# Optimization experiments

Hardware: AMD Instinct MI355X
Metric: run time of the kernel (lower is better)

The kernel has to match this reference:

```python
import jax, jax.numpy as jnp
import numpy as np

EPSILON = 0.1   # attention threshold
LN_EPS = 1e-5   # torch LayerNorm default
NORM_EPS = 1e-12  # torch F.normalize default


def setup_inputs() -> dict:
    key = jax.random.key(0)
    k1, k2, k3 = jax.random.split(key, 3)
    B, N, D = 4, 4096, 512
    Dqk, Dv = 512, 512
    x = jax.random.normal(k1, (B, N, D), dtype=jnp.float32)
    # xavier_uniform for Linear(in_dim, out_dim): bound = sqrt(6/(in+out))
    bqk = float(np.sqrt(6.0 / (D + Dqk)))
    bv = float(np.sqrt(6.0 / (D + Dv)))
    W_qk = jax.random.uniform(k2, (Dqk, D), minval=-bqk, maxval=bqk, dtype=jnp.float32)
    W_v = jax.random.uniform(k3, (Dv, D), minval=-bv, maxval=bv, dtype=jnp.float32)
    gamma = jnp.ones((Dv,), dtype=jnp.float32)
    beta = jnp.zeros((Dv,), dtype=jnp.float32)
    return {"x": x, "W_qk": W_qk, "W_v": W_v, "gamma": gamma, "beta": beta}


def reference(x, W_qk, W_v, gamma, beta):
    # q and k share the same projection (proj_qk applied twice to x)
    q = jnp.einsum('bnd,ed->bne', x, W_qk)   # [B,N,Dqk]
    v = jnp.einsum('bnd,ed->bne', x, W_v)    # [B,N,Dv]
    # L2 normalize (torch F.normalize: x / max(||x||, eps))
    qn = q / jnp.maximum(jnp.linalg.norm(q, axis=-1, keepdims=True), NORM_EPS)
    # cosine-similarity attention [B,N,N]
    attn = jnp.einsum('bne,bme->bnm', qn, qn)
    # epsilon-thresholded mask (detached in torch; constant here too)
    mask = jax.lax.stop_gradient((attn > EPSILON).astype(attn.dtype))
    attn = attn * mask  # markoff value is 0
    out = jnp.einsum('bnm,bme->bne', attn, v)  # [B,N,Dv]
    # LayerNorm over last dim
    mean = jnp.mean(out, axis=-1, keepdims=True)
    var = jnp.var(out, axis=-1, keepdims=True)
    out = (out - mean) * jax.lax.rsqrt(var + LN_EPS) * gamma + beta
    return out
```

## Files before the change

kernel.cpp:

```cpp
#include <hip/hip_runtime.h>
#include <hip/hip_bf16.h>
#include <stdint.h>


typedef __bf16 bf16;
typedef __bf16 bf16x8 __attribute__((ext_vector_type(8)));
typedef _Float16 f16;
typedef _Float16 f16x8 __attribute__((ext_vector_type(8)));
typedef unsigned short u16x8 __attribute__((ext_vector_type(8)));
typedef float f4 __attribute__((ext_vector_type(4)));
typedef float f16v __attribute__((ext_vector_type(16)));

#define CAP2 512
#define QBAND 2e-4f
#define BCAPC 512

#define SPLIT_HL(v0, v1, h, l)                                              \
    do {                                                                    \
        h[0] = (f16)v0.x; l[0] = (f16)((v0.x - (float)h[0]) * 2048.0f);     \
        h[1] = (f16)v0.y; l[1] = (f16)((v0.y - (float)h[1]) * 2048.0f);     \
        h[2] = (f16)v0.z; l[2] = (f16)((v0.z - (float)h[2]) * 2048.0f);     \
        h[3] = (f16)v0.w; l[3] = (f16)((v0.w - (float)h[3]) * 2048.0f);     \
        h[4] = (f16)v1.x; l[4] = (f16)((v1.x - (float)h[4]) * 2048.0f);     \
        h[5] = (f16)v1.y; l[5] = (f16)((v1.y - (float)h[5]) * 2048.0f);     \
        h[6] = (f16)v1.z; l[6] = (f16)((v1.z - (float)h[6]) * 2048.0f);     \
        h[7] = (f16)v1.w; l[7] = (f16)((v1.w - (float)h[7]) * 2048.0f);     \
    } while (0)

__global__ __launch_bounds__(512) void proj_q16(const float* __restrict__ X,
                                                const float* __restrict__ W,
                                                float* __restrict__ Q) {
    __shared__ f16 Bh[2][128][128];
    __shared__ f16 Bl[2][128][128];
    const int t = threadIdx.x;
    const int wave = t >> 6, lane = t & 63;
    const int ln16 = lane & 15, hi4 = lane >> 4;
    const int rg = wave >> 1, mg = wave & 1;
    const int n0 = blockIdx.x * 64;

    f16x8 Ah[16], Al[16];
    {
        const size_t arow = (size_t)(n0 + rg * 16 + ln16) * 512;
#pragma unroll
        for (int s = 0; s < 16; ++s) {
            f4 x0 = *(const f4*)&X[arow + s * 32 + hi4 * 8];
            f4 x1 = *(const f4*)&X[arow + s * 32 + hi4 * 8 + 4];
            f16x8 h, l;
            SPLIT_HL(x0, x1, h, l);
            Ah[s] = h; Al[s] = l;
        }
    }

#pragma unroll
    for (int i = 0; i < 4; ++i) {
        int id = i * 512 + t, r = id >> 4, s = id & 15;
        f4 w0 = *(const f4*)&W[(size_t)r * 512 + s * 8];
        f4 w1 = *(const f4*)&W[(size_t)r * 512 + s * 8 + 4];
        f16x8 h, l;
        SPLIT_HL(w0, w1, h, l);
        *(f16x8*)&Bh[0][r][(s ^ (r & 15)) * 8] = h;
        *(f16x8*)&Bl[0][r][(s ^ (r & 15)) * 8] = l;
    }
    __syncthreads();

    for (int ch = 0; ch < 4; ++ch) {
        const int eb = ch * 128;
        f4 Shh[4] = {}, Smid[4] = {};
#pragma unroll
        for (int k0i = 0; k0i < 4; ++k0i) {
            const int buf = k0i & 1;
            const bool last = (ch == 3) && (k0i == 3);
            const int neb = (k0i < 3) ? eb : eb + 128;
            const int nkb = (k0i < 3) ? (k0i + 1) * 128 : 0;
            f4 Lw[8];
            if (!last) {
#pragma unroll
                for (int i = 0; i < 4; ++i) {
                    int id = i * 512 + t, r = id >> 4, s = id & 15;
                    Lw[i * 2]     = *(const f4*)&W[(size_t)(neb + r) * 512 + nkb + s * 8];
                    Lw[i * 2 + 1] = *(const f4*)&W[(size_t)(neb + r) * 512 + nkb + s * 8 + 4];
                }
            }
#pragma unroll
            for (int kk = 0; kk < 4; ++kk) {
                const int s = k0i * 4 + kk;
                const f16x8 ah = Ah[s], al = Al[s];
#pragma unroll
                for (int tt = 0; tt < 4; ++tt) {
                    const int br = mg * 64 + tt * 16 + ln16;
                    const int sl = ((kk * 4 + hi4) ^ ln16) * 8;
                    f16x8 bh = *(const f16x8*)&Bh[buf][br][sl];
                    f16x8 bl = *(const f16x8*)&Bl[buf][br][sl];
                    Shh[tt]  = __builtin_amdgcn_mfma_f32_16x16x32_f16(ah, bh, Shh[tt], 0, 0, 0);
                    Smid[tt] = __builtin_amdgcn_mfma_f32_16x16x32_f16(al, bh, Smid[tt], 0, 0, 0);
                    Smid[tt] = __builtin_amdgcn_mfma_f32_16x16x32_f16(ah, bl, Smid[tt], 0, 0, 0);
                }
            }
            __syncthreads();
            if (!last) {
#pragma unroll
                for (int i = 0; i < 4; ++i) {
                    int id = i * 512 + t, r = id >> 4, s = id & 15;
                    f4 w0 = Lw[i * 2], w1 = Lw[i * 2 + 1];
                    f16x8 h, l;
                    SPLIT_HL(w0, w1, h, l);
                    *(f16x8*)&Bh[buf ^ 1][r][(s ^ (r & 15)) * 8] = h;
                    *(f16x8*)&Bl[buf ^ 1][r][(s ^ (r & 15)) * 8] = l;
                }
            }
            __syncthreads();
        }
#pragma unroll
        for (int tt = 0; tt < 4; ++tt) {
            const int ecol = eb + mg * 64 + tt * 16 + ln16;
#pragma unroll
            for (int i = 0; i < 4; ++i)
                Q[(size_t)(n0 + rg * 16 + hi4 * 4 + i) * 512 + ecol] =
                    Shh[tt][i] + Smid[tt][i] * (1.0f / 2048.0f);
        }
    }
}

__global__ __launch_bounds__(256) void proj_v16(const float* __restrict__ X,
                                                const float* __restrict__ W,
                                                bf16* __restrict__ VT) {
    __shared__ f16 Xs[128][256];
    const int t = threadIdx.x;
    const int wave = t >> 6, lane = t & 63;
    const int lo = lane & 15, h = lane >> 4;
    const int m0g = blockIdx.x * 128;
    const int e0 = blockIdx.y * 64;
    const int b = m0g >> 12, ml = m0g & 4095;

    f16x8 A[16];
    {
        const size_t arow = (size_t)(e0 + wave * 16 + lo) * 512;
#pragma unroll
        for (int s = 0; s < 16; ++s) {
            f4 w0 = *(const f4*)&W[arow + s * 32 + h * 8];
            f4 w1 = *(const f4*)&W[arow + s * 32 + h * 8 + 4];
            f16x8 a;
            a[0] = (f16)w0.x; a[1] = (f16)w0.y; a[2] = (f16)w0.z; a[3] = (f16)w0.w;
            a[4] = (f16)w1.x; a[5] = (f16)w1.y; a[6] = (f16)w1.z; a[7] = (f16)w1.w;
            A[s] = a;
        }
    }

    f4 acc[8] = {};
    for (int ph = 0; ph < 2; ++ph) {
        __syncthreads();
#pragma unroll
        for (int i = 0; i < 16; ++i) {
            int id = i * 256 + t;
            int r = id >> 5, s8 = id & 31;
            f4 x0 = *(const f4*)&X[(size_t)(m0g + r) * 512 + ph * 256 + s8 * 8];
            f4 x1 = *(const f4*)&X[(size_t)(m0g + r) * 512 + ph * 256 + s8 * 8 + 4];
            f16x8 v;
            v[0] = (f16)x0.x; v[1] = (f16)x0.y; v[2] = (f16)x0.z; v[3] = (f16)x0.w;
            v[4] = (f16)x1.x; v[5] = (f16)x1.y; v[6] = (f16)x1.z; v[7] = (f16)x1.w;
            int sl = (s8 & 16) | ((s8 ^ r) & 15);
            *(f16x8*)&Xs[r][sl * 8] = v;
        }
        __syncthreads();
#pragma unroll
        for (int s = 0; s < 8; ++s) {
            const f16x8 a = A[ph * 8 + s];
#pragma unroll
            for (int jt = 0; jt < 8; ++jt) {
                int rr = jt * 16 + lo;
                int c8 = s * 4 + h;
                int sl = (c8 & 16) | ((c8 ^ rr) & 15);
                f16x8 bb = *(const f16x8*)&Xs[rr][sl * 8];
                acc[jt] = __builtin_amdgcn_mfma_f32_16x16x32_f16(a, bb, acc[jt], 0, 0, 0);
            }
        }
    }
#pragma unroll
    for (int jt = 0; jt < 8; ++jt)
#pragma unroll
        for (int r = 0; r < 4; ++r) {
            int e = e0 + wave * 16 + h * 4 + r;
            int m = ml + jt * 16 + lo;
            VT[((size_t)b * 512 + e) * 4096 + m] = (bf16)acc[jt][r];
        }
}

__global__ __launch_bounds__(256) void norm_q(float* __restrict__ Q,
                                              f16* __restrict__ QH) {
    const int wave = threadIdx.x >> 6, lane = threadIdx.x & 63;
    const int row = blockIdx.x * 4 + wave;
    float* q = Q + (size_t)row * 512;
    float x[8];
    double s = 0.0;
    for (int j = 0; j < 8; ++j) { x[j] = q[lane * 8 + j]; s += (double)x[j] * x[j]; }
    for (int off = 1; off < 64; off <<= 1) s += __shfl_xor(s, off);
    double nm = fmax(sqrt(s), 1e-12);
    for (int j = 0; j < 8; ++j) {
        float qf = (float)((double)x[j] / nm);
        q[lane * 8 + j] = qf;
        QH[(size_t)row * 512 + lane * 8 + j] = (f16)qf;
    }
}

__global__ __launch_bounds__(512) void qk_mfma(const float* __restrict__ QF,
                                               const f16* __restrict__ QHB,
                                               uint16_t* __restrict__ counts,
                                               uint16_t* __restrict__ idxs,
                                               bf16* __restrict__ vals) {
    __shared__ f16 Bs[2][128][128];
    __shared__ int cnt[128];
    __shared__ int bcnt;
    __shared__ uint32_t blist[BCAPC];

    const int t = threadIdx.x;
    const int wave = t >> 6, lane = t & 63;
    const int ln16 = lane & 15, hi4 = lane >> 4;
    const int rg = wave >> 1, mg = wave & 1;
    const int grp = blockIdx.x & 7;
    const int b = grp >> 1, half = grp & 1;
    const int n0 = (blockIdx.x >> 3) * 128;
    const size_t nb = (size_t)b * 4096;
    const float* qf = QF + nb * 512;
    const f16* qh = QHB + nb * 512;
    const int mbase = half * 2048;

    f16x8 A[2][16];
#pragma unroll
    for (int rt = 0; rt < 2; ++rt) {
        const size_t arow = (size_t)(n0 + rg * 32 + rt * 16 + ln16) * 512;
#pragma unroll
        for (int s = 0; s < 16; ++s)
            A[rt][s] = *(const f16x8*)&qh[arow + s * 32 + hi4 * 8];
    }

    if (t < 128) cnt[t] = 0;
    if (t == 0) bcnt = 0;

#pragma unroll
    for (int i = 0; i < 4; ++i) {
        int id = i * 512 + t, r = id >> 4, s = id & 15;
        *(f16x8*)&Bs[0][r][(s ^ (r & 15)) * 8] =
            *(const f16x8*)&qh[(size_t)(mbase + r) * 512 + s * 8];
    }
    __syncthreads();

    for (int ch = 0; ch < 16; ++ch) {
        const int mst = mbase + ch * 128;
        f4 S[2][4] = {};
#pragma unroll
        for (int k0i = 0; k0i < 4; ++k0i) {
            const int buf = k0i & 1;
            const bool last = (k0i == 3) && (ch == 15);
            const int nmst = (k0i < 3) ? mst : mst + 128;
            const int nk0 = (k0i < 3) ? (k0i + 1) * 128 : 0;
            f16x8 L[4];
            if (!last) {
#pragma unroll
                for (int i = 0; i < 4; ++i) {
                    int id = i * 512 + t, r = id >> 4, s = id & 15;
                    L[i] = *(const f16x8*)&qh[(size_t)(nmst + r) * 512 + nk0 + s * 8];
                }
            }
#pragma unroll
            for (int kk = 0; kk < 4; ++kk) {
                const int s = k0i * 4 + kk;
                const f16x8 a0 = A[0][s], a1 = A[1][s];
#pragma unroll
                for (int tt = 0; tt < 4; ++tt) {
                    const int br = mg * 64 + tt * 16 + ln16;
                    f16x8 bb = *(const f16x8*)&Bs[buf][br][((kk * 4 + hi4) ^ ln16) * 8];
                    S[0][tt] = __builtin_amdgcn_mfma_f32_16x16x32_f16(a0, bb, S[0][tt], 0, 0, 0);
                    S[1][tt] = __builtin_amdgcn_mfma_f32_16x16x32_f16(a1, bb, S[1][tt], 0, 0, 0);
                }
            }
            if (k0i == 3) {
#pragma unroll
                for (int rt = 0; rt < 2; ++rt)
#pragma unroll
                    for (int tt = 0; tt < 4; ++tt) {
                        const int m = mst + mg * 64 + tt * 16 + ln16;
#pragma unroll
                        for (int i = 0; i < 4; ++i) {
                            float cs = S[rt][tt][i];
                            int row = rg * 32 + rt * 16 + hi4 * 4 + i;
                            if (cs > 0.1f + QBAND) {
                                int pos = atomicAdd(&cnt[row], 1);
                                if (pos < CAP2) {
                                    size_t o = ((size_t)(nb + n0 + row) * 2 + half) * CAP2 + pos;
                                    idxs[o] = (uint16_t)m;
                                    vals[o] = (bf16)cs;
                                }
                            } else if (cs > 0.1f - QBAND) {
                                int bp = atomicAdd(&bcnt, 1);
                                if (bp < BCAPC)
                                    blist[bp] = ((uint32_t)row << 12) | (uint32_t)m;
                            }
                        }
                    }
            }
            __syncthreads();
            if (!last) {
#pragma unroll
                for (int i = 0; i < 4; ++i) {
                    int id = i * 512 + t, r = id >> 4, s = id & 15;
                    *(f16x8*)&Bs[buf ^ 1][r][(s ^ (r & 15)) * 8] = L[i];
                }
            }
            if (k0i == 3) {
                int nbd = bcnt; if (nbd > BCAPC) nbd = BCAPC;
                for (int p = wave; p < nbd; p += 8) {
                    uint32_t pk = blist[p];
                    int row = (int)(pk >> 12), m = (int)(pk & 4095);
                    const float* qa = qf + (size_t)(n0 + row) * 512;
                    const float* qc = qf + (size_t)m * 512;
                    f4 a0 = *(const f4*)&qa[lane * 8];
                    f4 a1 = *(const f4*)&qa[lane * 8 + 4];
                    f4 c0 = *(const f4*)&qc[lane * 8];
                    f4 c1 = *(const f4*)&qc[lane * 8 + 4];
                    double s = (double)a0.x * c0.x + (double)a0.y * c0.y +
                               (double)a0.z * c0.z + (double)a0.w * c0.w +
                               (double)a1.x * c1.x + (double)a1.y * c1.y +
                               (double)a1.z * c1.z + (double)a1.w * c1.w;
                    for (int off = 1; off < 64; off <<= 1) s += __shfl_xor(s, off);
                    if (lane == 0 && s > 0.1) {
                        int pos = atomicAdd(&cnt[row], 1);
                        if (pos < CAP2) {
                            size_t o = ((size_t)(nb + n0 + row) * 2 + half) * CAP2 + pos;
                            idxs[o] = (uint16_t)m;
                            vals[o] = (bf16)(float)s;
                        }
                    }
                }
            }
            __syncthreads();
            if (k0i == 3 && t == 0) bcnt = 0;
        }
    }
    __syncthreads();
    if (t < 128) {
        int c = cnt[t];
        counts[(size_t)(nb + n0 + t) * 2 + half] = (uint16_t)(c > CAP2 ? CAP2 : c);
    }
}

__global__ __launch_bounds__(512, 2) void pv_mfma(const bf16* __restrict__ VT,
                                                  const uint16_t* __restrict__ counts,
                                                  const uint16_t* __restrict__ idxs,
                                                  const bf16* __restrict__ vals,
                                                  const float* __restrict__ gamma,
                                                  const float* __restrict__ beta,
                                                  float* __restrict__ Out) {
    __shared__ __align__(16) char smemraw[147456];
    bf16 (*Vts)[128] = (bf16(*)[128])smemraw;
    bf16 (*Wsm)[128] = (bf16(*)[128])(smemraw + 131072);

    const int t = threadIdx.x;
    const int wave = t >> 6, lane = t & 63;
    const int l31 = lane & 31, l15 = lane & 15, g = lane >> 5;
    const int grp = blockIdx.x & 7;
    const int b = grp >> 1;
    const int n0 = ((blockIdx.x >> 3) + ((grp & 1) ? 32 : 0)) * 64;
    const size_t nb = (size_t)b * 4096;
    const bf16* vtb = VT + (size_t)b * 512 * 4096;

    int myc0 = 0, myc1 = 0, cu = 0, pb = 0;
    u16x8 pi0 = {}, pi1 = {};
    bf16x8 pv0 = {}, pv1 = {};
    size_t base0 = 0, base1 = 0;
    if (t < 64) {
        myc0 = (int)counts[(size_t)(nb + n0 + t) * 2 + 0];
        myc1 = (int)counts[(size_t)(nb + n0 + t) * 2 + 1];
        if (myc0 > CAP2) myc0 = CAP2;
        if (myc1 > CAP2) myc1 = CAP2;
        base0 = ((size_t)(nb + n0 + t) * 2 + 0) * CAP2;
        base1 = ((size_t)(nb + n0 + t) * 2 + 1) * CAP2;
        pi0 = *(const u16x8*)&idxs[base0];
        pi1 = *(const u16x8*)&idxs[base0 + 8];
        pv0 = *(const bf16x8*)&vals[base0];
        pv1 = *(const bf16x8*)&vals[base0 + 8];
    }

    bf16x8 L[16];
#pragma unroll
    for (int i = 0; i < 16; ++i) {
        int id = i * 512 + t, r = id >> 4, s = id & 15;
        L[i] = *(const bf16x8*)&vtb[(size_t)r * 4096 + s * 8];
    }

    f16v acc[2][2] = {};

    for (int ch = 0; ch < 32; ++ch) {
        __syncthreads();
#pragma unroll
        for (int i = 0; i < 16; ++i) {
            int id = i * 512 + t, r = id >> 4, s = id & 15;
            *(bf16x8*)&Vts[r][(s ^ (r & 15)) << 3] = L[i];
        }
        if (t < 64) {
            bf16 z0 = (bf16)0.0f;
            bf16x8 zv = {z0, z0, z0, z0, z0, z0, z0, z0};
#pragma unroll
            for (int sj = 0; sj < 16; ++sj) *(bf16x8*)&Wsm[t][sj * 8] = zv;
            if (ch == 16) cu = 0;
            const int m0l = ch * 128;
            const int myc = (ch >= 16) ? myc1 : myc0;
            const size_t base = (ch >= 16) ? base1 : base0;
            int end = cu;
#pragma unroll
            for (int j = 0; j < 16; ++j) {
                int pos = pb + j;
                int mi = (j < 8) ? (int)pi0[j] : (int)pi1[j - 8];
                bf16 vv = (j < 8) ? pv0[j] : pv1[j - 8];
                if (pos == end && pos < myc && mi < m0l + 128) {
                    int lo = mi - m0l;
                    Wsm[t][(((lo >> 3) ^ (t & 15)) << 3) | (lo & 7)] = vv;
                    end = pos + 1;
                }
            }
            if (end == pb + 16) {
                while (end < myc) {
                    int mi = (int)idxs[base + end];
                    if (mi >= m0l + 128) break;
                    int lo = mi - m0l;
                    Wsm[t][(((lo >> 3) ^ (t & 15)) << 3) | (lo & 7)] =
                        vals[base + end];
                    ++end;
                }
            }
            cu = end;
        }
        __syncthreads();
        if (ch < 31) {
            const int mo = (ch + 1) * 128;
#pragma unroll
            for (int i = 0; i < 16; ++i) {
                int id = i * 512 + t, r = id >> 4, s = id & 15;
                L[i] = *(const bf16x8*)&vtb[(size_t)r * 4096 + mo + s * 8];
            }
            if (t < 64) {
                int ncu = (ch + 1 == 16) ? 0 : cu;
                const size_t nbase = (ch + 1 >= 16) ? base1 : base0;
                pb = ncu & ~7;
                pi0 = *(const u16x8*)&idxs[nbase + pb];
                pi1 = *(const u16x8*)&idxs[nbase + pb + 8];
                pv0 = *(const bf16x8*)&vals[nbase + pb];
                pv1 = *(const bf16x8*)&vals[nbase + pb + 8];
            }
        }
#pragma unroll
        for (int ks = 0; ks < 8; ++ks) {
            const int sw = (((ks * 2 + g) ^ l15) << 3);
            bf16x8 A0 = *(const bf16x8*)&Wsm[l31][sw];
            bf16x8 A1 = *(const bf16x8*)&Wsm[32 + l31][sw];
            bf16x8 B0 = *(const bf16x8*)&Vts[wave * 64 + l31][sw];
            bf16x8 B1 = *(const bf16x8*)&Vts[wave * 64 + 32 + l31][sw];
            acc[0][0] = __builtin_amdgcn_mfma_f32_32x32x16_bf16(A0, B0, acc[0][0], 0, 0, 0);
            acc[0][1] = __builtin_amdgcn_mfma_f32_32x32x16_bf16(A0, B1, acc[0][1], 0, 0, 0);
            acc[1][0] = __builtin_amdgcn_mfma_f32_32x32x16_bf16(A1, B0, acc[1][0], 0, 0, 0);
            acc[1][1] = __builtin_amdgcn_mfma_f32_32x32x16_bf16(A1, B1, acc[1][1], 0, 0, 0);
        }
    }

    __syncthreads();
    float* red = (float*)smemraw;
    float* mrs = (float*)(smemraw + 4096);
#pragma unroll
    for (int nt = 0; nt < 2; ++nt)
#pragma unroll
        for (int r = 0; r < 16; ++r) {
            float v0 = acc[nt][0][r], v1 = acc[nt][1][r];
            float s = v0 + v1, q = v0 * v0 + v1 * v1;
            for (int off = 1; off < 32; off <<= 1) {
                s += __shfl_xor(s, off);
                q += __shfl_xor(q, off);
            }
            if (l31 == 0) {
                int nloc = nt * 32 + (r & 3) + 8 * (r >> 2) + 4 * g;
                red[(wave * 64 + nloc) * 2] = s;
                red[(wave * 64 + nloc) * 2 + 1] = q;
            }
        }
    __syncthreads();
    if (t < 64) {
        float s = 0.f, q = 0.f;
        for (int w2 = 0; w2 < 8; ++w2) {
            s += red[(w2 * 64 + t) * 2];
            q += red[(w2 * 64 + t) * 2 + 1];
        }
        float mu = s * (1.0f / 512.0f);
        float var = q * (1.0f / 512.0f) - mu * mu;
        mrs[t] = mu;
        mrs[64 + t] = rsqrtf(var + 1e-5f);
    }
    __syncthreads();
    const float g0 = gamma[wave * 64 + l31], g1 = gamma[wave * 64 + 32 + l31];
    const float b0 = beta[wave * 64 + l31], b1 = beta[wave * 64 + 32 + l31];
#pragma unroll
    for (int nt = 0; nt < 2; ++nt)
#pragma unroll
        for (int r = 0; r < 16; ++r) {
            int nloc = nt * 32 + (r & 3) + 8 * (r >> 2) + 4 * g;
            float mu = mrs[nloc], rs = mrs[64 + nloc];
            size_t ro = (nb + n0 + nloc) * 512;
            float y0 = (acc[nt][0][r] - mu) * rs * g0 + b0;
            float y1 = (acc[nt][1][r] - mu) * rs * g1 + b1;
            Out[ro + wave * 64 + l31] = y0;
            Out[ro + wave * 64 + 32 + l31] = y1;
        }
}

extern "C" void kernel_launch(void* const* d_in, const int* in_sizes, int n_in,
                              void* d_out, int out_size, void* d_ws, size_t ws_size,
                              hipStream_t stream) {
    const float* x     = (const float*)d_in[0];
    const float* wqk   = (const float*)d_in[1];
    const float* wv    = (const float*)d_in[2];
    const float* gamma = (const float*)d_in[3];
    const float* beta  = (const float*)d_in[4];
    float* out = (float*)d_out;

    char* ws = (char*)d_ws;
    uint16_t* idxs   = (uint16_t*)ws;
    bf16*     vals   = (bf16*)(ws + 33554432);
    float*    qn32   = (float*)(ws + 67108864);
    f16*      qh16   = (f16*)(ws + 100663296);
    bf16*     vt     = (bf16*)(ws + 134217728);
    uint16_t* counts = (uint16_t*)(ws + 150994944);
    const size_t need = 151060480;
    if (ws_size < need) return;

    proj_q16<<<256, 512, 0, stream>>>(x, wqk, qn32);
    proj_v16<<<dim3(128, 8), 256, 0, stream>>>(x, wv, vt);
    norm_q<<<4096, 256, 0, stream>>>(qn32, qh16);
    qk_mfma<<<256, 512, 0, stream>>>(qn32, qh16, counts, idxs, vals);
    pv_mfma<<<256, 512, 0, stream>>>(vt, counts, idxs, vals, gamma, beta, out);
}
```

Baseline: 490.0 us.

## Split PV kernel across output-column halves and finish LayerNorm in separate kernel

The PV kernel now launches twice as many blocks, each computing only half of the 512 output columns for a 64-row tile, which halves the shared-memory footprint and the V tile loads per block. Partial row sums and sums of squares go to a workspace buffer, and a new ln_fin kernel combines them and applies the LayerNorm. The aim is more parallelism and better occupancy on the many-CU GPU. In exchange, each block redoes the sparse weight tile construction, and the unnormalised output takes an extra round trip through global memory plus one more kernel launch.

```diff
diff --git a/kernel.cpp b/kernel.cpp
--- a/kernel.cpp
+++ b/kernel.cpp
@@ -343,25 +343,25 @@
     }
 }
 
-__global__ __launch_bounds__(512, 2) void pv_mfma(const bf16* __restrict__ VT,
-                                                  const uint16_t* __restrict__ counts,
-                                                  const uint16_t* __restrict__ idxs,
-                                                  const bf16* __restrict__ vals,
-                                                  const float* __restrict__ gamma,
-                                                  const float* __restrict__ beta,
-                                                  float* __restrict__ Out) {
-    __shared__ __align__(16) char smemraw[147456];
+__global__ __launch_bounds__(512) void pv_mfma(const bf16* __restrict__ VT,
+                                               const uint16_t* __restrict__ counts,
+                                               const uint16_t* __restrict__ idxs,
+                                               const bf16* __restrict__ vals,
+                                               float* __restrict__ O,
+                                               float* __restrict__ sums) {
+    __shared__ __align__(16) char smemraw[81920];
     bf16 (*Vts)[128] = (bf16(*)[128])smemraw;
-    bf16 (*Wsm)[128] = (bf16(*)[128])(smemraw + 131072);
+    bf16 (*Wsm)[128] = (bf16(*)[128])(smemraw + 65536);
 
     const int t = threadIdx.x;
     const int wave = t >> 6, lane = t & 63;
     const int l31 = lane & 31, l15 = lane & 15, g = lane >> 5;
     const int grp = blockIdx.x & 7;
-    const int b = grp >> 1;
-    const int n0 = ((blockIdx.x >> 3) + ((grp & 1) ? 32 : 0)) * 64;
+    const int b = grp >> 1, eh = grp & 1;
+    const int n0 = (blockIdx.x >> 3) * 64;
+    const int e0 = eh * 256;
     const size_t nb = (size_t)b * 4096;
-    const bf16* vtb = VT + (size_t)b * 512 * 4096;
+    const bf16* vtb = VT + ((size_t)b * 512 + e0) * 4096;
 
     int myc0 = 0, myc1 = 0, cu = 0, pb = 0;
     u16x8 pi0 = {}, pi1 = {};
@@ -380,19 +380,20 @@
         pv1 = *(const bf16x8*)&vals[base0 + 8];
     }
 
-    bf16x8 L[16];
-#pragma unroll
-    for (int i = 0; i < 16; ++i) {
+    bf16x8 L[8];
+#pragma unroll
+    for (int i = 0; i < 8; ++i) {
         int id = i * 512 + t, r = id >> 4, s = id & 15;
         L[i] = *(const bf16x8*)&vtb[(size_t)r * 4096 + s * 8];
     }
 
-    f16v acc[2][2] = {};
+    const int nt = wave & 1, q = wave >> 1;
+    f16v acc[2] = {};
 
     for (int ch = 0; ch < 32; ++ch) {
         __syncthreads();
 #pragma unroll
-        for (int i = 0; i < 16; ++i) {
+        for (int i = 0; i < 8; ++i) {
             int id = i * 512 + t, r = id >> 4, s = id & 15;
             *(bf16x8*)&Vts[r][(s ^ (r & 15)) << 3] = L[i];
         }
@@ -433,7 +434,7 @@
         if (ch < 31) {
             const int mo = (ch + 1) * 128;
 #pragma unroll
-            for (int i = 0; i < 16; ++i) {
+            for (int i = 0; i < 8; ++i) {
                 int id = i * 512 + t, r = id >> 4, s = id & 15;
                 L[i] = *(const bf16x8*)&vtb[(size_t)r * 4096 + mo + s * 8];
             }
@@ -450,63 +451,74 @@
 #pragma unroll
         for (int ks = 0; ks < 8; ++ks) {
             const int sw = (((ks * 2 + g) ^ l15) << 3);
-            bf16x8 A0 = *(const bf16x8*)&Wsm[l31][sw];
-            bf16x8 A1 = *(const bf16x8*)&Wsm[32 + l31][sw];
-            bf16x8 B0 = *(const bf16x8*)&Vts[wave * 64 + l31][sw];
-            bf16x8 B1 = *(const bf16x8*)&Vts[wave * 64 + 32 + l31][sw];
-            acc[0][0] = __builtin_amdgcn_mfma_f32_32x32x16_bf16(A0, B0, acc[0][0], 0, 0, 0);
-            acc[0][1] = __builtin_amdgcn_mfma_f32_32x32x16_bf16(A0, B1, acc[0][1], 0, 0, 0);
-            acc[1][0] = __builtin_amdgcn_mfma_f32_32x32x16_bf16(A1, B0, acc[1][0], 0, 0, 0);
-            acc[1][1] = __builtin_amdgcn_mfma_f32_32x32x16_bf16(A1, B1, acc[1][1], 0, 0, 0);
+            bf16x8 A0 = *(const bf16x8*)&Wsm[nt * 32 + l31][sw];
+            bf16x8 B0 = *(const bf16x8*)&Vts[q * 64 + l31][sw];
+            bf16x8 B1 = *(const bf16x8*)&Vts[q * 64 + 32 + l31][sw];
+            acc[0] = __builtin_amdgcn_mfma_f32_32x32x16_bf16(A0, B0, acc[0], 0, 0, 0);
+            acc[1] = __builtin_amdgcn_mfma_f32_32x32x16_bf16(A0, B1, acc[1], 0, 0, 0);
         }
     }
 
     __syncthreads();
     float* red = (float*)smemraw;
-    float* mrs = (float*)(smemraw + 4096);
-#pragma unroll
-    for (int nt = 0; nt < 2; ++nt)
-#pragma unroll
-        for (int r = 0; r < 16; ++r) {
-            float v0 = acc[nt][0][r], v1 = acc[nt][1][r];
-            float s = v0 + v1, q = v0 * v0 + v1 * v1;
-            for (int off = 1; off < 32; off <<= 1) {
-                s += __shfl_xor(s, off);
-                q += __shfl_xor(q, off);
-            }
-            if (l31 == 0) {
-                int nloc = nt * 32 + (r & 3) + 8 * (r >> 2) + 4 * g;
-                red[(wave * 64 + nloc) * 2] = s;
-                red[(wave * 64 + nloc) * 2 + 1] = q;
-            }
-        }
+#pragma unroll
+    for (int r = 0; r < 16; ++r) {
+        float v0 = acc[0][r], v1 = acc[1][r];
+        float s = v0 + v1, qq = v0 * v0 + v1 * v1;
+        for (int off = 1; off < 32; off <<= 1) {
+            s += __shfl_xor(s, off);
+            qq += __shfl_xor(qq, off);
+        }
+        if (l31 == 0) {
+            int nloc = nt * 32 + (r & 3) + 8 * (r >> 2) + 4 * g;
+            red[(q * 64 + nloc) * 2] = s;
+            red[(q * 64 + nloc) * 2 + 1] = qq;
+        }
+    }
     __syncthreads();
     if (t < 64) {
-        float s = 0.f, q = 0.f;
-        for (int w2 = 0; w2 < 8; ++w2) {
-            s += red[(w2 * 64 + t) * 2];
-            q += red[(w2 * 64 + t) * 2 + 1];
-        }
-        float mu = s * (1.0f / 512.0f);
-        float var = q * (1.0f / 512.0f) - mu * mu;
-        mrs[t] = mu;
-        mrs[64 + t] = rsqrtf(var + 1e-5f);
-    }
-    __syncthreads();
-    const float g0 = gamma[wave * 64 + l31], g1 = gamma[wave * 64 + 32 + l31];
-    const float b0 = beta[wave * 64 + l31], b1 = beta[wave * 64 + 32 + l31];
-#pragma unroll
-    for (int nt = 0; nt < 2; ++nt)
+        float s = red[t * 2] + red[(64 + t) * 2] + red[(128 + t) * 2] + red[(192 + t) * 2];
+        float qq = red[t * 2 + 1] + red[(64 + t) * 2 + 1] + red[(128 + t) * 2 + 1] + red[(192 + t) * 2 + 1];
+        size_t so = ((size_t)(nb + n0 + t) * 2 + eh) * 2;
+        sums[so] = s;
+        sums[so + 1] = qq;
+    }
+#pragma unroll
+    for (int s2 = 0; s2 < 2; ++s2)
 #pragma unroll
         for (int r = 0; r < 16; ++r) {
             int nloc = nt * 32 + (r & 3) + 8 * (r >> 2) + 4 * g;
-            float mu = mrs[nloc], rs = mrs[64 + nloc];
-            size_t ro = (nb + n0 + nloc) * 512;
-            float y0 = (acc[nt][0][r] - mu) * rs * g0 + b0;
-            float y1 = (acc[nt][1][r] - mu) * rs * g1 + b1;
-            Out[ro + wave * 64 + l31] = y0;
-            Out[ro + wave * 64 + 32 + l31] = y1;
-        }
+            int col = e0 + q * 64 + s2 * 32 + l31;
+            O[(nb + n0 + nloc) * 512 + col] = acc[s2][r];
+        }
+}
+
+__global__ __launch_bounds__(256) void ln_fin(const float* __restrict__ O,
+                                              const float* __restrict__ sums,
+                                              const float* __restrict__ gamma,
+                                              const float* __restrict__ beta,
+                                              float* __restrict__ Out) {
+    const int wave = threadIdx.x >> 6, lane = threadIdx.x & 63;
+    const size_t row = (size_t)blockIdx.x * 4 + wave;
+    float s = sums[row * 4 + 0] + sums[row * 4 + 2];
+    float qq = sums[row * 4 + 1] + sums[row * 4 + 3];
+    float mu = s * (1.0f / 512.0f);
+    float var = qq * (1.0f / 512.0f) - mu * mu;
+    float rs = rsqrtf(var + 1e-5f);
+    const float* o = O + row * 512;
+    float* out = Out + row * 512;
+#pragma unroll
+    for (int j2 = 0; j2 < 2; ++j2) {
+        const int c = lane * 8 + j2 * 4;
+        f4 v = *(const f4*)&o[c];
+        f4 gm = *(const f4*)&gamma[c];
+        f4 bt = *(const f4*)&beta[c];
+        v.x = (v.x - mu) * rs * gm.x + bt.x;
+        v.y = (v.y - mu) * rs * gm.y + bt.y;
+        v.z = (v.z - mu) * rs * gm.z + bt.z;
+        v.w = (v.w - mu) * rs * gm.w + bt.w;
+        *(f4*)&out[c] = v;
+    }
 }
 
 extern "C" void kernel_launch(void* const* d_in, const int* in_sizes, int n_in,
@@ -524,8 +536,10 @@
     bf16*     vals   = (bf16*)(ws + 33554432);
     float*    qn32   = (float*)(ws + 67108864);
     f16*      qh16   = (f16*)(ws + 100663296);
+    float*    sums   = (float*)(ws + 117440512);
     bf16*     vt     = (bf16*)(ws + 134217728);
     uint16_t* counts = (uint16_t*)(ws + 150994944);
+    float*    obuf   = (float*)(ws + 67108864);
     const size_t need = 151060480;
     if (ws_size < need) return;
 
@@ -533,5 +547,6 @@
     proj_v16<<<dim3(128, 8), 256, 0, stream>>>(x, wv, vt);
     norm_q<<<4096, 256, 0, stream>>>(qn32, qh16);
     qk_mfma<<<256, 512, 0, stream>>>(qn32, qh16, counts, idxs, vals);
-    pv_mfma<<<256, 512, 0, stream>>>(vt, counts, idxs, vals, gamma, beta, out);
-}
+    pv_mfma<<<512, 512, 0, stream>>>(vt, counts, idxs, vals, obuf, sums);
+    ln_fin<<<4096, 256, 0, stream>>>(obuf, sums, gamma, beta, out);
+}
```

After: 573.8 us. 17.1% more time.
